# Kernel tuning notes

Measured on AMD Instinct MI355X. Metric: run time of the kernel, lower is better.

## Reference

```python
import jax, jax.numpy as jnp
import numpy as np

B, D, K = 32, 64, 256            # batch, num objects (seq len), feature size (== in_size)
G = [256, 256, 256]              # g_layers sizes
F1, F2, OUT = 256, 256, 128      # f_fc1, f_fc2, out_size


def setup_inputs() -> dict:
    key = jax.random.key(0)
    ks = jax.random.split(key, 16)
    scale = 0.02

    def w(k, shape):
        return jax.random.normal(k, shape, dtype=jnp.float32) * scale

    x = jax.random.normal(ks[0], (B, D, K), dtype=jnp.float32)
    # edge_feature: Linear(2*K, K). Stored [in, out] (transposed vs torch).
    edge_w = w(ks[1], (2 * K, K))
    edge_b = jnp.zeros((K,), dtype=jnp.float32)
    g_ws, g_bs = [], []
    in_s = K
    for i, out_s in enumerate(G):
        g_ws.append(w(ks[2 + i], (in_s, out_s)))
        g_bs.append(jnp.zeros((out_s,), dtype=jnp.float32))
        in_s = out_s
    f1_w = w(ks[8], (G[-1], F1)); f1_b = jnp.zeros((F1,), dtype=jnp.float32)
    f2_w = w(ks[9], (F1, F2));    f2_b = jnp.zeros((F2,), dtype=jnp.float32)
    f3_w = w(ks[10], (F2, OUT));  f3_b = jnp.zeros((OUT,), dtype=jnp.float32)
    return dict(x=x, edge_w=edge_w, edge_b=edge_b, g_ws=g_ws, g_bs=g_bs,
                f1_w=f1_w, f1_b=f1_b, f2_w=f2_w, f2_b=f2_b, f3_w=f3_w, f3_b=f3_b)


def reference(x, edge_w, edge_b, g_ws, g_bs, f1_w, f1_b, f2_w, f2_b, f3_w, f3_b):
    # x: [B, D, K]. Original builds x_full[b,i,j] = concat(x[b,j], x[b,i]) then
    # applies edge_feature (Linear(2K -> K)). Equivalent, without materializing the
    # concat: split edge_w into the halves acting on x_i (=x[b,j]) and x_j (=x[b,i]).
    k = x.shape[-1]
    u = x @ edge_w[:k]      # [B, D, K]  -> indexed by j (axis 2)
    v = x @ edge_w[k:]      # [B, D, K]  -> indexed by i (axis 1)
    h = u[:, None, :, :] + v[:, :, None, :] + edge_b   # [B, D, D, K]
    # g MLP over all d^2 pairs (Linear + ReLU chain)
    for gw, gb in zip(g_ws, g_bs):
        h = jax.nn.relu(h @ gw + gb)
    # sum-aggregate over all pairs
    x_g = h.sum(axis=(1, 2))                            # [B, G[-1]]
    # f MLP (dropout p=0.0 -> identity)
    x_f = jax.nn.relu(x_g @ f1_w + f1_b)
    x_f = jax.nn.relu(x_f @ f2_w + f2_b)
    return x_f @ f3_w + f3_b                            # [B, OUT]
```

## Files before the change

kernel.cpp:

```cpp
#include <hip/hip_runtime.h>
#include <hip/hip_bf16.h>

typedef __attribute__((ext_vector_type(4))) float f32x4;
typedef __attribute__((ext_vector_type(2))) int   i32x2;
typedef __attribute__((ext_vector_type(4))) int   i32x4;
typedef __attribute__((ext_vector_type(8))) short short8;

__device__ __forceinline__ unsigned short f2bf(float x) {
  __hip_bfloat16 h = __float2bfloat16(x);
  union { __hip_bfloat16 h1; unsigned short u; } c; c.h1 = h; return c.u;
}
__device__ __forceinline__ unsigned pk2(float a, float b) {
  __hip_bfloat162 h = __float22bfloat162_rn(make_float2(a, b));
  union { __hip_bfloat162 h2; unsigned u; } c; c.h2 = h; return c.u;
}
__device__ __forceinline__ float bf2f(unsigned short u) {
  union { unsigned u32; float f; } c; c.u32 = ((unsigned)u) << 16; return c.f;
}

__global__ void k_prep(const float* __restrict__ edge_w, const float* __restrict__ edge_b,
                       const float* __restrict__ gw0, const float* __restrict__ gb0,
                       const float* __restrict__ gw1, const float* __restrict__ gw2,
                       float* __restrict__ W1u, float* __restrict__ W1v,
                       float* __restrict__ c1,
                       unsigned short* __restrict__ W2R, unsigned short* __restrict__ W3R) {
  const int blk = blockIdx.x, t = threadIdx.x;
  __shared__ float eu[256], ev[256];
  if (blk < 256) {
    eu[t] = edge_w[blk * 256 + t];
    ev[t] = edge_w[(256 + blk) * 256 + t];
    __syncthreads();
    float su = 0.f, sv = 0.f;
    for (int o = 0; o < 256; ++o) {
      float gg = gw0[o * 256 + t];
      su += eu[o] * gg; sv += ev[o] * gg;
    }
    W1u[blk * 256 + t] = su;
    W1v[blk * 256 + t] = sv;
  } else if (blk == 256) {
    float s = gb0[t];
    for (int o = 0; o < 256; ++o) s += edge_b[o] * gw0[o * 256 + t];
    c1[t] = s;
  } else {
    int p = blk - 257;
    const float* src = (p < 32) ? gw1 : gw2;
    unsigned short* dst = (p < 32) ? W2R : W3R;
    p &= 31;
    int w = p >> 3, ch = p & 7;
    int mf = t >> 6, lane = t & 63, q = lane & 15, g = lane >> 4;
    int base = ((w * 8 + ch) * 4 + mf) * 512 + lane * 8;
    int m = w * 64 + mf * 16 + q;
#pragma unroll
    for (int e = 0; e < 8; ++e) {
      int k = ch * 32 + g * 8 + e;
      dst[base + e] = f2bf(src[k * 256 + m]);
    }
  }
}

__global__ void k_wcvt(const float* __restrict__ W1u, const float* __restrict__ W1v,
                       unsigned short* __restrict__ W1uR, unsigned short* __restrict__ W1vR) {
  int p = blockIdx.x;
  const float* src = (p < 32) ? W1u : W1v;
  unsigned short* dst = (p < 32) ? W1uR : W1vR;
  p &= 31;
  const int t = threadIdx.x;
  int w = p >> 3, ch = p & 7;
  int mf = t >> 6, lane = t & 63, q = lane & 15, g = lane >> 4;
  int base = ((w * 8 + ch) * 4 + mf) * 512 + lane * 8;
  int m = w * 64 + mf * 16 + q;
#pragma unroll
  for (int e = 0; e < 8; ++e) {
    int k = ch * 32 + g * 8 + e;
    dst[base + e] = f2bf(src[k * 256 + m]);
  }
}

__global__ void k_uv(const float* __restrict__ x,
                     const unsigned short* __restrict__ W1uR,
                     const unsigned short* __restrict__ W1vR,
                     const float* __restrict__ c1,
                     unsigned short* __restrict__ U1, float* __restrict__ V1c) {
  __shared__ unsigned short xs[8192];

  const int t = threadIdx.x;
  const int tile = blockIdx.x >> 1, sel = blockIdx.x & 1;
  const int r0 = tile * 32;
  const int wid = t >> 6, lane = t & 63;
  const int q = lane & 15, g = lane >> 4;
  const int mo = wid << 6;

  {
    const int row = t >> 3, sl = t & 7, r7 = row & 7;
    const float* xB = x + (size_t)(r0 + row) * 256;
    unsigned short* hB = xs + row * 256;
#pragma unroll
    for (int m = 0; m < 4; ++m) {
      int ks = sl + 8 * m;
      f32x4 u0 = *(const f32x4*)(xB + ks * 8);
      f32x4 u1 = *(const f32x4*)(xB + ks * 8 + 4);
      i32x4 wv = { (int)pk2(u0.x, u0.y), (int)pk2(u0.z, u0.w),
                   (int)pk2(u1.x, u1.y), (int)pk2(u1.z, u1.w) };
      *(i32x4*)(hB + (ks ^ r7) * 8) = wv;
    }
  }

  const unsigned short* WR = sel ? W1vR : W1uR;
  const unsigned short* aW = WR + (size_t)wid * 16384 + lane * 8;

  short8 a_[4], an_[4];
#pragma unroll
  for (int mf = 0; mf < 4; ++mf) a_[mf] = *(const short8*)(aW + mf * 512);

  __syncthreads();

  f32x4 acc[4][2];
#pragma unroll
  for (int mf = 0; mf < 4; ++mf)
#pragma unroll
    for (int nf = 0; nf < 2; ++nf) acc[mf][nf] = (f32x4){0.f, 0.f, 0.f, 0.f};

  for (int ch = 0; ch < 8; ++ch) {
    if (ch < 7) {
#pragma unroll
      for (int mf = 0; mf < 4; ++mf)
        an_[mf] = *(const short8*)(aW + (ch + 1) * 2048 + mf * 512);
    }
    short8 b_[2];
#pragma unroll
    for (int nf = 0; nf < 2; ++nf) {
      int r = q + 16 * nf;
      b_[nf] = *(const short8*)(xs + r * 256 + (((ch * 4 + g) ^ (r & 7)) * 8));
    }
#pragma unroll
    for (int mf = 0; mf < 4; ++mf)
#pragma unroll
      for (int nf = 0; nf < 2; ++nf)
        acc[mf][nf] = __builtin_amdgcn_mfma_f32_16x16x32_bf16(a_[mf], b_[nf], acc[mf][nf], 0, 0, 0);
    if (ch < 7) {
#pragma unroll
      for (int mf = 0; mf < 4; ++mf) a_[mf] = an_[mf];
    }
  }

#pragma unroll
  for (int mf = 0; mf < 4; ++mf) {
    int c2b = mo + 16 * mf + 4 * g;
#pragma unroll
    for (int nf = 0; nf < 2; ++nf) {
      int r = r0 + q + 16 * nf;
      f32x4 v = acc[mf][nf];
      if (sel == 0) {
        i32x2 wv = { (int)pk2(v.x, v.y), (int)pk2(v.z, v.w) };
        *(i32x2*)(U1 + (size_t)r * 256 + c2b) = wv;
      } else {
        f32x4 cc = *(const f32x4*)(c1 + c2b);
        f32x4 o = { v.x + cc.x, v.y + cc.y, v.z + cc.z, v.w + cc.w };
        *(f32x4*)(V1c + (size_t)r * 256 + c2b) = o;
      }
    }
  }
}

__device__ __forceinline__ void write_h1(short8 u, f32x4 v0, f32x4 v1,
                                         unsigned short* dst) {
  float r0 = fmaxf(bf2f((unsigned short)u[0]) + v0.x, 0.f);
  float r1 = fmaxf(bf2f((unsigned short)u[1]) + v0.y, 0.f);
  float r2 = fmaxf(bf2f((unsigned short)u[2]) + v0.z, 0.f);
  float r3 = fmaxf(bf2f((unsigned short)u[3]) + v0.w, 0.f);
  float r4 = fmaxf(bf2f((unsigned short)u[4]) + v1.x, 0.f);
  float r5 = fmaxf(bf2f((unsigned short)u[5]) + v1.y, 0.f);
  float r6 = fmaxf(bf2f((unsigned short)u[6]) + v1.z, 0.f);
  float r7 = fmaxf(bf2f((unsigned short)u[7]) + v1.w, 0.f);
  i32x4 wv = { (int)pk2(r0, r1), (int)pk2(r2, r3), (int)pk2(r4, r5), (int)pk2(r6, r7) };
  *(i32x4*)dst = wv;
}

__launch_bounds__(256, 3)
__global__ void k_main(const unsigned short* __restrict__ U1,
                       const float* __restrict__ V1c,
                       const unsigned short* __restrict__ W2R,
                       const unsigned short* __restrict__ W3R,
                       const float* __restrict__ b2, const float* __restrict__ b3,
                       float* __restrict__ partials) {
  __shared__ unsigned short hbuf[16384];

  const int t = threadIdx.x;
  const int bid = blockIdx.x;
  const int wrk = ((bid & 7) << 8) | (bid >> 3);
  const int b = wrk >> 6;
  const int wid = t >> 6, lane = t & 63;
  const int q = lane & 15, g = lane >> 4;
  const int mo = wid << 6;

  {
    const int row = t >> 2, sl = t & 3, r7 = row & 7;
    const unsigned short* uB = U1 + (size_t)(b * 64 + row) * 256;
    const float* vB = V1c + (size_t)wrk * 256;
    unsigned short* hB = hbuf + row * 256;
#pragma unroll
    for (int m = 0; m < 8; ++m) {
      int ks = sl + 4 * m;
      int s = ks ^ r7;
      short8 u = *(const short8*)(uB + ks * 8);
      f32x4 v0 = *(const f32x4*)(vB + ks * 8);
      f32x4 v1 = *(const f32x4*)(vB + ks * 8 + 4);
      write_h1(u, v0, v1, hB + s * 8);
    }
  }

  const unsigned short* aW2 = W2R + (size_t)wid * 16384 + lane * 8;
  const unsigned short* aW3 = W3R + (size_t)wid * 16384 + lane * 8;

  short8 a_[4], an_[4];
#pragma unroll
  for (int mf = 0; mf < 4; ++mf) a_[mf] = *(const short8*)(aW2 + mf * 512);

  __syncthreads();

  f32x4 acc[4][4];
#pragma unroll
  for (int mf = 0; mf < 4; ++mf)
#pragma unroll
    for (int nf = 0; nf < 4; ++nf) acc[mf][nf] = (f32x4){0.f, 0.f, 0.f, 0.f};

  for (int ch = 0; ch < 8; ++ch) {
    if (ch < 7) {
#pragma unroll
      for (int mf = 0; mf < 4; ++mf)
        an_[mf] = *(const short8*)(aW2 + (ch + 1) * 2048 + mf * 512);
    }
    short8 b_[4];
#pragma unroll
    for (int nf = 0; nf < 4; ++nf) {
      int r = q + 16 * nf;
      b_[nf] = *(const short8*)(hbuf + r * 256 + (((ch * 4 + g) ^ (r & 7)) * 8));
    }
#pragma unroll
    for (int mf = 0; mf < 4; ++mf)
#pragma unroll
      for (int nf = 0; nf < 4; ++nf)
        acc[mf][nf] = __builtin_amdgcn_mfma_f32_16x16x32_bf16(a_[mf], b_[nf], acc[mf][nf], 0, 0, 0);
    if (ch < 7) {
#pragma unroll
      for (int mf = 0; mf < 4; ++mf) a_[mf] = an_[mf];
    }
  }

  __syncthreads();

#pragma unroll
  for (int mf = 0; mf < 4; ++mf) a_[mf] = *(const short8*)(aW3 + mf * 512);
#pragma unroll
  for (int mf = 0; mf < 4; ++mf) {
    int c2b = mo + 16 * mf + 4 * g;
    f32x4 bb = *(const f32x4*)(b2 + c2b);
    int ksw = c2b >> 3, off = c2b & 7;
#pragma unroll
    for (int nf = 0; nf < 4; ++nf) {
      int r = q + 16 * nf;
      f32x4 v = acc[mf][nf];
      float e0 = fmaxf(v.x + bb.x, 0.f), e1 = fmaxf(v.y + bb.y, 0.f);
      float e2 = fmaxf(v.z + bb.z, 0.f), e3 = fmaxf(v.w + bb.w, 0.f);
      i32x2 wv = { (int)pk2(e0, e1), (int)pk2(e2, e3) };
      *(i32x2*)(hbuf + r * 256 + ((ksw ^ (r & 7)) * 8) + off) = wv;
    }
  }
  __syncthreads();

  f32x4 acc2[4][4];
#pragma unroll
  for (int mf = 0; mf < 4; ++mf)
#pragma unroll
    for (int nf = 0; nf < 4; ++nf) acc2[mf][nf] = (f32x4){0.f, 0.f, 0.f, 0.f};

  for (int ch = 0; ch < 8; ++ch) {
    if (ch < 7) {
#pragma unroll
      for (int mf = 0; mf < 4; ++mf)
        an_[mf] = *(const short8*)(aW3 + (ch + 1) * 2048 + mf * 512);
    }
    short8 b_[4];
#pragma unroll
    for (int nf = 0; nf < 4; ++nf) {
      int r = q + 16 * nf;
      b_[nf] = *(const short8*)(hbuf + r * 256 + (((ch * 4 + g) ^ (r & 7)) * 8));
    }
#pragma unroll
    for (int mf = 0; mf < 4; ++mf)
#pragma unroll
      for (int nf = 0; nf < 4; ++nf)
        acc2[mf][nf] = __builtin_amdgcn_mfma_f32_16x16x32_bf16(a_[mf], b_[nf], acc2[mf][nf], 0, 0, 0);
    if (ch < 7) {
#pragma unroll
      for (int mf = 0; mf < 4; ++mf) a_[mf] = an_[mf];
    }
  }

  __syncthreads();

  float* scr = (float*)&hbuf[0];
#pragma unroll
  for (int mf = 0; mf < 4; ++mf) {
    int n3b = mo + 16 * mf + 4 * g;
    f32x4 bb = *(const f32x4*)(b3 + n3b);
    f32x4 sum = (f32x4){0.f, 0.f, 0.f, 0.f};
#pragma unroll
    for (int nf = 0; nf < 4; ++nf) {
      f32x4 v = acc2[mf][nf];
      sum.x += fmaxf(v.x + bb.x, 0.f);
      sum.y += fmaxf(v.y + bb.y, 0.f);
      sum.z += fmaxf(v.z + bb.z, 0.f);
      sum.w += fmaxf(v.w + bb.w, 0.f);
    }
    *(f32x4*)(scr + q * 264 + n3b) = sum;
  }
  __syncthreads();
  float s = 0.f;
#pragma unroll
  for (int q2 = 0; q2 < 16; ++q2) s += scr[q2 * 264 + t];
  partials[(size_t)wrk * 256 + t] = s;
}

__global__ void k_fmlp(const float* __restrict__ partials,
                       const float* __restrict__ f1w, const float* __restrict__ f1b,
                       const float* __restrict__ f2w, const float* __restrict__ f2b,
                       const float* __restrict__ f3w, const float* __restrict__ f3b,
                       float* __restrict__ out) {
  const int b = blockIdx.x, t = threadIdx.x;
  __shared__ float xg[256], x1[256], x2[256];
  {
    const float* p = partials + (size_t)(b * 64) * 256 + t;
    float s[8];
#pragma unroll
    for (int i = 0; i < 8; ++i) s[i] = 0.f;
#pragma unroll
    for (int k = 0; k < 8; ++k)
#pragma unroll
      for (int i = 0; i < 8; ++i) s[i] += p[(k * 8 + i) * 256];
    float tot = 0.f;
#pragma unroll
    for (int i = 0; i < 8; ++i) tot += s[i];
    xg[t] = tot;
  }
  __syncthreads();
  {
    float a0 = 0.f, a1 = 0.f, a2 = 0.f, a3 = 0.f;
#pragma unroll 4
    for (int k = 0; k < 64; ++k) {
      a0 += xg[k]       * f1w[(k)       * 256 + t];
      a1 += xg[k + 64]  * f1w[(k + 64)  * 256 + t];
      a2 += xg[k + 128] * f1w[(k + 128) * 256 + t];
      a3 += xg[k + 192] * f1w[(k + 192) * 256 + t];
    }
    x1[t] = fmaxf((a0 + a1) + (a2 + a3) + f1b[t], 0.f);
  }
  __syncthreads();
  {
    float a0 = 0.f, a1 = 0.f, a2 = 0.f, a3 = 0.f;
#pragma unroll 4
    for (int k = 0; k < 64; ++k) {
      a0 += x1[k]       * f2w[(k)       * 256 + t];
      a1 += x1[k + 64]  * f2w[(k + 64)  * 256 + t];
      a2 += x1[k + 128] * f2w[(k + 128) * 256 + t];
      a3 += x1[k + 192] * f2w[(k + 192) * 256 + t];
    }
    x2[t] = fmaxf((a0 + a1) + (a2 + a3) + f2b[t], 0.f);
  }
  __syncthreads();
  if (t < 128) {
    float a0 = 0.f, a1 = 0.f, a2 = 0.f, a3 = 0.f;
#pragma unroll 4
    for (int k = 0; k < 64; ++k) {
      a0 += x2[k]       * f3w[(k)       * 128 + t];
      a1 += x2[k + 64]  * f3w[(k + 64)  * 128 + t];
      a2 += x2[k + 128] * f3w[(k + 128) * 128 + t];
      a3 += x2[k + 192] * f3w[(k + 192) * 128 + t];
    }
    out[b * 128 + t] = (a0 + a1) + (a2 + a3) + f3b[t];
  }
}

__global__ void k_zero(float* __restrict__ out, int n) {
  int i = blockIdx.x * 256 + threadIdx.x;
  if (i < n) out[i] = 0.f;
}

extern "C" void kernel_launch(void* const* d_in, const int* in_sizes, int n_in,
                              void* d_out, int out_size, void* d_ws, size_t ws_size,
                              hipStream_t stream) {
  const float* x      = (const float*)d_in[0];
  const float* edge_w = (const float*)d_in[1];
  const float* edge_b = (const float*)d_in[2];
  const float *gw0, *gw1, *gw2, *gb0, *gb1, *gb2;
  const float *f1w, *f1b, *f2w, *f2b, *f3w, *f3b;

  if (n_in >= 15 && in_sizes[3] == 65536 && in_sizes[4] == 65536 && in_sizes[5] == 65536) {
    gw0 = (const float*)d_in[3]; gw1 = (const float*)d_in[4]; gw2 = (const float*)d_in[5];
    gb0 = (const float*)d_in[6]; gb1 = (const float*)d_in[7]; gb2 = (const float*)d_in[8];
    f1w = (const float*)d_in[9];  f1b = (const float*)d_in[10];
    f2w = (const float*)d_in[11]; f2b = (const float*)d_in[12];
    f3w = (const float*)d_in[13]; f3b = (const float*)d_in[14];
  } else if (n_in >= 15 && in_sizes[3] == 65536 && in_sizes[4] == 256) {
    gw0 = (const float*)d_in[3]; gb0 = (const float*)d_in[4];
    gw1 = (const float*)d_in[5]; gb1 = (const float*)d_in[6];
    gw2 = (const float*)d_in[7]; gb2 = (const float*)d_in[8];
    f1w = (const float*)d_in[9];  f1b = (const float*)d_in[10];
    f2w = (const float*)d_in[11]; f2b = (const float*)d_in[12];
    f3w = (const float*)d_in[13]; f3b = (const float*)d_in[14];
  } else {
    const float* gws = (const float*)d_in[3];
    const float* gbs = (const float*)d_in[4];
    gw0 = gws;          gw1 = gws + 65536;  gw2 = gws + 131072;
    gb0 = gbs;          gb1 = gbs + 256;    gb2 = gbs + 512;
    f1w = (const float*)d_in[5];  f1b = (const float*)d_in[6];
    f2w = (const float*)d_in[7];  f2b = (const float*)d_in[8];
    f3w = (const float*)d_in[9];  f3b = (const float*)d_in[10];
  }

  char* ws = (char*)d_ws;
  float*          W1u      = (float*)(ws);
  float*          W1v      = (float*)(ws + 262144);
  float*          c1       = (float*)(ws + 524288);
  unsigned short* W2R      = (unsigned short*)(ws + 525312);
  unsigned short* W3R      = (unsigned short*)(ws + 656384);
  unsigned short* U1       = (unsigned short*)(ws + 787456);
  float*          V1c      = (float*)(ws + 1836032);
  float*          partials = (float*)(ws + 3933184);
  unsigned short* W1uR     = (unsigned short*)(ws + 3933184);
  unsigned short* W1vR     = (unsigned short*)(ws + 3933184 + 131072);
  const size_t need = 6030336;
  (void)out_size; (void)n_in;

  if (ws_size < need) {
    k_zero<<<dim3((out_size + 255) / 256), dim3(256), 0, stream>>>((float*)d_out, out_size);
    return;
  }

  k_prep<<<dim3(321), dim3(256), 0, stream>>>(edge_w, edge_b, gw0, gb0, gw1, gw2,
                                              W1u, W1v, c1, W2R, W3R);
  k_wcvt<<<dim3(64), dim3(256), 0, stream>>>(W1u, W1v, W1uR, W1vR);
  k_uv<<<dim3(128), dim3(256), 0, stream>>>(x, W1uR, W1vR, c1, U1, V1c);
  k_main<<<dim3(2048), dim3(256), 0, stream>>>(U1, V1c, W2R, W3R, gb1, gb2, partials);
  k_fmlp<<<dim3(32), dim3(256), 0, stream>>>(partials, f1w, f1b, f2w, f2b, f3w, f3b,
                                             (float*)d_out);
}
```

Baseline: 76.04 us.

## Process two i-rows per k_main block and fuse W1 bf16 relayout into k_prep

Each k_main block now computes two pair-rows (two V vectors sharing the same U tile), so every weight A-fragment loaded from global memory feeds twice as many MFMAs. The grid halves to 1024 blocks, LDS doubles to two 32 KB buffers, and launch bounds drop from 3 to 2 waves per SIMD to leave room for the doubled accumulators. Separately, k_prep writes W1u/W1v directly in the swizzled bf16 layout, which removes the k_wcvt launch and the fp32 intermediate buffers. The tradeoff is lower occupancy and higher register pressure in k_main, in exchange for halved weight traffic per unit of work.

```diff
diff --git a/kernel.cpp b/kernel.cpp
--- a/kernel.cpp
+++ b/kernel.cpp
@@ -21,7 +21,7 @@
 __global__ void k_prep(const float* __restrict__ edge_w, const float* __restrict__ edge_b,
                        const float* __restrict__ gw0, const float* __restrict__ gb0,
                        const float* __restrict__ gw1, const float* __restrict__ gw2,
-                       float* __restrict__ W1u, float* __restrict__ W1v,
+                       unsigned short* __restrict__ W1uR, unsigned short* __restrict__ W1vR,
                        float* __restrict__ c1,
                        unsigned short* __restrict__ W2R, unsigned short* __restrict__ W3R) {
   const int blk = blockIdx.x, t = threadIdx.x;
@@ -35,8 +35,12 @@
       float gg = gw0[o * 256 + t];
       su += eu[o] * gg; sv += ev[o] * gg;
     }
-    W1u[blk * 256 + t] = su;
-    W1v[blk * 256 + t] = sv;
+    const int k = blk, m = t;
+    const int w = m >> 6, mf = (m >> 4) & 3, q = m & 15;
+    const int ch = k >> 5, g = (k >> 3) & 3, e = k & 7;
+    const int idx = ((w * 8 + ch) * 4 + mf) * 512 + (g * 16 + q) * 8 + e;
+    W1uR[idx] = f2bf(su);
+    W1vR[idx] = f2bf(sv);
   } else if (blk == 256) {
     float s = gb0[t];
     for (int o = 0; o < 256; ++o) s += edge_b[o] * gw0[o * 256 + t];
@@ -58,24 +62,6 @@
   }
 }
 
-__global__ void k_wcvt(const float* __restrict__ W1u, const float* __restrict__ W1v,
-                       unsigned short* __restrict__ W1uR, unsigned short* __restrict__ W1vR) {
-  int p = blockIdx.x;
-  const float* src = (p < 32) ? W1u : W1v;
-  unsigned short* dst = (p < 32) ? W1uR : W1vR;
-  p &= 31;
-  const int t = threadIdx.x;
-  int w = p >> 3, ch = p & 7;
-  int mf = t >> 6, lane = t & 63, q = lane & 15, g = lane >> 4;
-  int base = ((w * 8 + ch) * 4 + mf) * 512 + lane * 8;
-  int m = w * 64 + mf * 16 + q;
-#pragma unroll
-  for (int e = 0; e < 8; ++e) {
-    int k = ch * 32 + g * 8 + e;
-    dst[base + e] = f2bf(src[k * 256 + m]);
-  }
-}
-
 __global__ void k_uv(const float* __restrict__ x,
                      const unsigned short* __restrict__ W1uR,
                      const unsigned short* __restrict__ W1vR,
@@ -176,19 +162,21 @@
   *(i32x4*)dst = wv;
 }
 
-__launch_bounds__(256, 3)
+__launch_bounds__(256, 2)
 __global__ void k_main(const unsigned short* __restrict__ U1,
                        const float* __restrict__ V1c,
                        const unsigned short* __restrict__ W2R,
                        const unsigned short* __restrict__ W3R,
                        const float* __restrict__ b2, const float* __restrict__ b3,
                        float* __restrict__ partials) {
-  __shared__ unsigned short hbuf[16384];
+  __shared__ unsigned short bufA[16384];
+  __shared__ unsigned short bufB[16384];
 
   const int t = threadIdx.x;
   const int bid = blockIdx.x;
-  const int wrk = ((bid & 7) << 8) | (bid >> 3);
-  const int b = wrk >> 6;
+  const int wrk = ((bid & 7) << 7) | (bid >> 3);
+  const int b = wrk >> 5;
+  const int it0 = (wrk & 31) * 2;
   const int wid = t >> 6, lane = t & 63;
   const int q = lane & 15, g = lane >> 4;
   const int mo = wid << 6;
@@ -196,16 +184,21 @@
   {
     const int row = t >> 2, sl = t & 3, r7 = row & 7;
     const unsigned short* uB = U1 + (size_t)(b * 64 + row) * 256;
-    const float* vB = V1c + (size_t)wrk * 256;
-    unsigned short* hB = hbuf + row * 256;
+    const float* vA = V1c + (size_t)(b * 64 + it0) * 256;
+    const float* vB = vA + 256;
+    unsigned short* dA = bufA + row * 256;
+    unsigned short* dB = bufB + row * 256;
 #pragma unroll
     for (int m = 0; m < 8; ++m) {
       int ks = sl + 4 * m;
-      int s = ks ^ r7;
+      int s8 = (ks ^ r7) * 8;
       short8 u = *(const short8*)(uB + ks * 8);
-      f32x4 v0 = *(const f32x4*)(vB + ks * 8);
-      f32x4 v1 = *(const f32x4*)(vB + ks * 8 + 4);
-      write_h1(u, v0, v1, hB + s * 8);
+      f32x4 a0 = *(const f32x4*)(vA + ks * 8);
+      f32x4 a1 = *(const f32x4*)(vA + ks * 8 + 4);
+      f32x4 b0 = *(const f32x4*)(vB + ks * 8);
+      f32x4 b1 = *(const f32x4*)(vB + ks * 8 + 4);
+      write_h1(u, a0, a1, dA + s8);
+      write_h1(u, b0, b1, dB + s8);
     }
   }
 
@@ -218,11 +211,14 @@
 
   __syncthreads();
 
-  f32x4 acc[4][4];
+  f32x4 accA[4][4], accB[4][4];
 #pragma unroll
   for (int mf = 0; mf < 4; ++mf)
 #pragma unroll
-    for (int nf = 0; nf < 4; ++nf) acc[mf][nf] = (f32x4){0.f, 0.f, 0.f, 0.f};
+    for (int nf = 0; nf < 4; ++nf) {
+      accA[mf][nf] = (f32x4){0.f, 0.f, 0.f, 0.f};
+      accB[mf][nf] = (f32x4){0.f, 0.f, 0.f, 0.f};
+    }
 
   for (int ch = 0; ch < 8; ++ch) {
     if (ch < 7) {
@@ -230,17 +226,21 @@
       for (int mf = 0; mf < 4; ++mf)
         an_[mf] = *(const short8*)(aW2 + (ch + 1) * 2048 + mf * 512);
     }
-    short8 b_[4];
+    short8 bA[4], bB[4];
 #pragma unroll
     for (int nf = 0; nf < 4; ++nf) {
       int r = q + 16 * nf;
-      b_[nf] = *(const short8*)(hbuf + r * 256 + (((ch * 4 + g) ^ (r & 7)) * 8));
+      int off = r * 256 + (((ch * 4 + g) ^ (r & 7)) * 8);
+      bA[nf] = *(const short8*)(bufA + off);
+      bB[nf] = *(const short8*)(bufB + off);
     }
 #pragma unroll
     for (int mf = 0; mf < 4; ++mf)
 #pragma unroll
-      for (int nf = 0; nf < 4; ++nf)
-        acc[mf][nf] = __builtin_amdgcn_mfma_f32_16x16x32_bf16(a_[mf], b_[nf], acc[mf][nf], 0, 0, 0);
+      for (int nf = 0; nf < 4; ++nf) {
+        accA[mf][nf] = __builtin_amdgcn_mfma_f32_16x16x32_bf16(a_[mf], bA[nf], accA[mf][nf], 0, 0, 0);
+        accB[mf][nf] = __builtin_amdgcn_mfma_f32_16x16x32_bf16(a_[mf], bB[nf], accB[mf][nf], 0, 0, 0);
+      }
     if (ch < 7) {
 #pragma unroll
       for (int mf = 0; mf < 4; ++mf) a_[mf] = an_[mf];
@@ -259,20 +259,26 @@
 #pragma unroll
     for (int nf = 0; nf < 4; ++nf) {
       int r = q + 16 * nf;
-      f32x4 v = acc[mf][nf];
-      float e0 = fmaxf(v.x + bb.x, 0.f), e1 = fmaxf(v.y + bb.y, 0.f);
-      float e2 = fmaxf(v.z + bb.z, 0.f), e3 = fmaxf(v.w + bb.w, 0.f);
-      i32x2 wv = { (int)pk2(e0, e1), (int)pk2(e2, e3) };
-      *(i32x2*)(hbuf + r * 256 + ((ksw ^ (r & 7)) * 8) + off) = wv;
-    }
-  }
-  __syncthreads();
-
-  f32x4 acc2[4][4];
+      int dst = r * 256 + ((ksw ^ (r & 7)) * 8) + off;
+      f32x4 vA_ = accA[mf][nf];
+      f32x4 vB_ = accB[mf][nf];
+      i32x2 wA = { (int)pk2(fmaxf(vA_.x + bb.x, 0.f), fmaxf(vA_.y + bb.y, 0.f)),
+                   (int)pk2(fmaxf(vA_.z + bb.z, 0.f), fmaxf(vA_.w + bb.w, 0.f)) };
+      i32x2 wB = { (int)pk2(fmaxf(vB_.x + bb.x, 0.f), fmaxf(vB_.y + bb.y, 0.f)),
+                   (int)pk2(fmaxf(vB_.z + bb.z, 0.f), fmaxf(vB_.w + bb.w, 0.f)) };
+      *(i32x2*)(bufA + dst) = wA;
+      *(i32x2*)(bufB + dst) = wB;
+    }
+  }
+  __syncthreads();
+
 #pragma unroll
   for (int mf = 0; mf < 4; ++mf)
 #pragma unroll
-    for (int nf = 0; nf < 4; ++nf) acc2[mf][nf] = (f32x4){0.f, 0.f, 0.f, 0.f};
+    for (int nf = 0; nf < 4; ++nf) {
+      accA[mf][nf] = (f32x4){0.f, 0.f, 0.f, 0.f};
+      accB[mf][nf] = (f32x4){0.f, 0.f, 0.f, 0.f};
+    }
 
   for (int ch = 0; ch < 8; ++ch) {
     if (ch < 7) {
@@ -280,17 +286,21 @@
       for (int mf = 0; mf < 4; ++mf)
         an_[mf] = *(const short8*)(aW3 + (ch + 1) * 2048 + mf * 512);
     }
-    short8 b_[4];
+    short8 bA[4], bB[4];
 #pragma unroll
     for (int nf = 0; nf < 4; ++nf) {
       int r = q + 16 * nf;
-      b_[nf] = *(const short8*)(hbuf + r * 256 + (((ch * 4 + g) ^ (r & 7)) * 8));
+      int off = r * 256 + (((ch * 4 + g) ^ (r & 7)) * 8);
+      bA[nf] = *(const short8*)(bufA + off);
+      bB[nf] = *(const short8*)(bufB + off);
     }
 #pragma unroll
     for (int mf = 0; mf < 4; ++mf)
 #pragma unroll
-      for (int nf = 0; nf < 4; ++nf)
-        acc2[mf][nf] = __builtin_amdgcn_mfma_f32_16x16x32_bf16(a_[mf], b_[nf], acc2[mf][nf], 0, 0, 0);
+      for (int nf = 0; nf < 4; ++nf) {
+        accA[mf][nf] = __builtin_amdgcn_mfma_f32_16x16x32_bf16(a_[mf], bA[nf], accA[mf][nf], 0, 0, 0);
+        accB[mf][nf] = __builtin_amdgcn_mfma_f32_16x16x32_bf16(a_[mf], bB[nf], accB[mf][nf], 0, 0, 0);
+      }
     if (ch < 7) {
 #pragma unroll
       for (int mf = 0; mf < 4; ++mf) a_[mf] = an_[mf];
@@ -299,27 +309,35 @@
 
   __syncthreads();
 
-  float* scr = (float*)&hbuf[0];
+  float* scrA = (float*)&bufA[0];
+  float* scrB = (float*)&bufB[0];
 #pragma unroll
   for (int mf = 0; mf < 4; ++mf) {
     int n3b = mo + 16 * mf + 4 * g;
     f32x4 bb = *(const f32x4*)(b3 + n3b);
-    f32x4 sum = (f32x4){0.f, 0.f, 0.f, 0.f};
-#pragma unroll
-    for (int nf = 0; nf < 4; ++nf) {
-      f32x4 v = acc2[mf][nf];
-      sum.x += fmaxf(v.x + bb.x, 0.f);
-      sum.y += fmaxf(v.y + bb.y, 0.f);
-      sum.z += fmaxf(v.z + bb.z, 0.f);
-      sum.w += fmaxf(v.w + bb.w, 0.f);
-    }
-    *(f32x4*)(scr + q * 264 + n3b) = sum;
-  }
-  __syncthreads();
-  float s = 0.f;
-#pragma unroll
-  for (int q2 = 0; q2 < 16; ++q2) s += scr[q2 * 264 + t];
-  partials[(size_t)wrk * 256 + t] = s;
+    f32x4 sA = (f32x4){0.f, 0.f, 0.f, 0.f};
+    f32x4 sB = (f32x4){0.f, 0.f, 0.f, 0.f};
+#pragma unroll
+    for (int nf = 0; nf < 4; ++nf) {
+      f32x4 vA_ = accA[mf][nf];
+      f32x4 vB_ = accB[mf][nf];
+      sA.x += fmaxf(vA_.x + bb.x, 0.f); sA.y += fmaxf(vA_.y + bb.y, 0.f);
+      sA.z += fmaxf(vA_.z + bb.z, 0.f); sA.w += fmaxf(vA_.w + bb.w, 0.f);
+      sB.x += fmaxf(vB_.x + bb.x, 0.f); sB.y += fmaxf(vB_.y + bb.y, 0.f);
+      sB.z += fmaxf(vB_.z + bb.z, 0.f); sB.w += fmaxf(vB_.w + bb.w, 0.f);
+    }
+    *(f32x4*)(scrA + q * 264 + n3b) = sA;
+    *(f32x4*)(scrB + q * 264 + n3b) = sB;
+  }
+  __syncthreads();
+  float sA = 0.f, sB = 0.f;
+#pragma unroll
+  for (int q2 = 0; q2 < 16; ++q2) {
+    sA += scrA[q2 * 264 + t];
+    sB += scrB[q2 * 264 + t];
+  }
+  partials[(size_t)(b * 64 + it0) * 256 + t] = sA;
+  partials[(size_t)(b * 64 + it0 + 1) * 256 + t] = sB;
 }
 
 __global__ void k_fmlp(const float* __restrict__ partials,
@@ -419,17 +437,15 @@
   }
 
   char* ws = (char*)d_ws;
-  float*          W1u      = (float*)(ws);
-  float*          W1v      = (float*)(ws + 262144);
-  float*          c1       = (float*)(ws + 524288);
-  unsigned short* W2R      = (unsigned short*)(ws + 525312);
-  unsigned short* W3R      = (unsigned short*)(ws + 656384);
-  unsigned short* U1       = (unsigned short*)(ws + 787456);
-  float*          V1c      = (float*)(ws + 1836032);
-  float*          partials = (float*)(ws + 3933184);
-  unsigned short* W1uR     = (unsigned short*)(ws + 3933184);
-  unsigned short* W1vR     = (unsigned short*)(ws + 3933184 + 131072);
-  const size_t need = 6030336;
+  float*          c1       = (float*)(ws);
+  unsigned short* W1uR     = (unsigned short*)(ws + 1024);
+  unsigned short* W1vR     = (unsigned short*)(ws + 132096);
+  unsigned short* W2R      = (unsigned short*)(ws + 263168);
+  unsigned short* W3R      = (unsigned short*)(ws + 394240);
+  unsigned short* U1       = (unsigned short*)(ws + 525312);
+  float*          V1c      = (float*)(ws + 1573888);
+  float*          partials = (float*)(ws + 3671040);
+  const size_t need = 5768192;
   (void)out_size; (void)n_in;
 
   if (ws_size < need) {
@@ -438,10 +454,9 @@
   }
 
   k_prep<<<dim3(321), dim3(256), 0, stream>>>(edge_w, edge_b, gw0, gb0, gw1, gw2,
-                                              W1u, W1v, c1, W2R, W3R);
-  k_wcvt<<<dim3(64), dim3(256), 0, stream>>>(W1u, W1v, W1uR, W1vR);
+                                              W1uR, W1vR, c1, W2R, W3R);
   k_uv<<<dim3(128), dim3(256), 0, stream>>>(x, W1uR, W1vR, c1, U1, V1c);
-  k_main<<<dim3(2048), dim3(256), 0, stream>>>(U1, V1c, W2R, W3R, gb1, gb2, partials);
+  k_main<<<dim3(1024), dim3(256), 0, stream>>>(U1, V1c, W2R, W3R, gb1, gb2, partials);
   k_fmlp<<<dim3(32), dim3(256), 0, stream>>>(partials, f1w, f1b, f2w, f2b, f3w, f3b,
                                              (float*)d_out);
 }
```

Measured after the change: 71.73 us. -5.7%, faster.
